# Kernel tuning notes

Hardware: AMD Instinct MI355X
Metric: run time of the kernel (lower is better)

The kernel has to match this reference:

```python
import jax, jax.numpy as jnp
import numpy as np

N_NODES = 50000
N_EDGES = 640000
D_IN = 128
D_HID = 128
D_OUT = 128
N_GRAPHS = 64


def gcn_conv(x, edge_index, W, b, n_nodes):
    """PyG GCNConv: D^{-1/2} (A + I) D^{-1/2} X W + b (unit edge weights)."""
    src, dst = edge_index[0], edge_index[1]
    h = x @ W  # [N, d_out]
    # degree counts target-side edges plus the self loop
    deg = jax.ops.segment_sum(jnp.ones_like(dst, dtype=h.dtype), dst,
                              num_segments=n_nodes) + 1.0
    dinv = jax.lax.rsqrt(deg)  # deg >= 1 so always finite
    norm = dinv[src] * dinv[dst]  # [E]
    msg = h[src] * norm[:, None]  # gather + scale  [E, d_out]
    agg = jax.ops.segment_sum(msg, dst, num_segments=n_nodes)
    # self-loop contribution: norm_ii = dinv_i^2
    agg = agg + h * (dinv * dinv)[:, None]
    return agg + b


def global_mean_pool(x, batch, n_graphs):
    sums = jax.ops.segment_sum(x, batch, num_segments=n_graphs)
    cnt = jax.ops.segment_sum(jnp.ones((x.shape[0],), dtype=x.dtype), batch,
                              num_segments=n_graphs)
    return sums / jnp.maximum(cnt, 1.0)[:, None]


def setup_inputs() -> dict:
    key = jax.random.key(0)
    k = jax.random.split(key, 8)
    x = jax.random.normal(k[0], (N_NODES, D_IN), dtype=jnp.float32)
    edge_index = jax.random.randint(k[1], (2, N_EDGES), 0, N_NODES, dtype=jnp.int64)
    batch = jnp.sort(jax.random.randint(k[2], (N_NODES,), 0, N_GRAPHS, dtype=jnp.int64))
    s1 = 1.0 / np.sqrt(D_IN)
    s2 = 1.0 / np.sqrt(D_HID)
    W1 = jax.random.uniform(k[3], (D_IN, D_HID), jnp.float32, -s1, s1)
    b1 = jnp.zeros((D_HID,), jnp.float32)
    W2 = jax.random.uniform(k[4], (D_HID, D_OUT), jnp.float32, -s2, s2)
    b2 = jnp.zeros((D_OUT,), jnp.float32)
    return {"x": x, "edge_index": edge_index, "batch": batch,
            "W1": W1, "b1": b1, "W2": W2, "b2": b2}


def reference(x, edge_index, batch, W1, b1, W2, b2):
    n = x.shape[0]
    h = jax.nn.relu(gcn_conv(x, edge_index, W1, b1, n))
    h = gcn_conv(h, edge_index, W2, b2, n)
    return global_mean_pool(h, batch, N_GRAPHS)
```

## Files before the change

kernel.cpp:

```cpp
#include <hip/hip_runtime.h>


#define D 128
#define NGRAPH 64
#define SCAN_B 1024
#define AGG_BLOCKS 2048

typedef _Float16 h16x2 __attribute__((ext_vector_type(2)));
typedef _Float16 f16x8 __attribute__((ext_vector_type(8)));
typedef float    f32x4 __attribute__((ext_vector_type(4)));

__device__ __forceinline__ float2 h2f(unsigned u) {
    h16x2 h = __builtin_bit_cast(h16x2, u);
    return make_float2((float)h.x, (float)h.y);
}
__device__ __forceinline__ unsigned f2h(float x, float y) {
    h16x2 h;
    h.x = (_Float16)x;
    h.y = (_Float16)y;
    return __builtin_bit_cast(unsigned, h);
}

__global__ void zero_out_kernel(float* __restrict__ out, int n) {
    int i = blockIdx.x * blockDim.x + threadIdx.x;
    if (i < n) out[i] = 0.f;
}

__global__ __launch_bounds__(256) void conv_count_kernel(const float* __restrict__ X,
                                                         _Float16* __restrict__ Xh,
                                                         const float* __restrict__ W1,
                                                         _Float16* __restrict__ WB,
                                                         const int* __restrict__ ei,
                                                         int* __restrict__ deg,
                                                         int N, int E, int cb) {
    int b = (int)blockIdx.x;
    if (b < cb) {
        int idx = b * 256 + (int)threadIdx.x;
        int total = N * (D / 4);
        if (idx < total) {
            float4 v = ((const float4*)X)[idx];
            uint2 o;
            o.x = f2h(v.x, v.y);
            o.y = f2h(v.z, v.w);
            ((uint2*)Xh)[idx] = o;
        }
        return;
    }
    if (b < cb + 8) {
        int idx = (b - cb) * 256 + (int)threadIdx.x;
        int lane = idx & 63;
        int nt   = (idx >> 6) & 7;
        int kt   = idx >> 9;
        int col  = nt * 16 + (lane & 15);
        int krow = kt * 32 + (lane >> 4) * 8;
#pragma unroll
        for (int j = 0; j < 8; ++j)
            WB[idx * 8 + j] = (_Float16)W1[(krow + j) * D + col];
        return;
    }
    int e = (b - cb - 8) * 256 + (int)threadIdx.x;
    if (e < E) {
        int d = ei[E + e];
        if (d >= 0 && d < N) atomicAdd(&deg[d], 1);
    }
}

__global__ __launch_bounds__(SCAN_B) void block_scan_kernel(const int* __restrict__ deg,
                                                            int* __restrict__ rowstart,
                                                            int* __restrict__ bsum,
                                                            float* __restrict__ dinv,
                                                            int N) {
    __shared__ int sc[SCAN_B];
    int t = threadIdx.x;
    int i = blockIdx.x * SCAN_B + t;
    int orig = (i < N) ? deg[i] : 0;
    int v = orig;
    sc[t] = v;
    __syncthreads();
    for (int off = 1; off < SCAN_B; off <<= 1) {
        int add = (t >= off) ? sc[t - off] : 0;
        __syncthreads();
        v += add;
        sc[t] = v;
        __syncthreads();
    }
    if (i < N) {
        rowstart[i] = v - orig;
        dinv[i]     = rsqrtf((float)orig + 1.0f);
    }
    if (t == SCAN_B - 1) bsum[blockIdx.x] = v;
}

__global__ __launch_bounds__(SCAN_B) void finalize_scan_kernel(const int* __restrict__ bsum,
                                                               int* __restrict__ rowstart,
                                                               int* __restrict__ cursor,
                                                               int N, int nblk, int E) {
    __shared__ int s_off;
    if (threadIdx.x < 64) {
        int lane = (int)threadIdx.x;
        int v = (lane < nblk && lane < (int)blockIdx.x) ? bsum[lane] : 0;
        for (int off = 32; off > 0; off >>= 1) v += __shfl_down(v, off);
        if (lane == 0) s_off = v;
    }
    __syncthreads();
    int i = blockIdx.x * SCAN_B + threadIdx.x;
    if (i < N) {
        int rs = rowstart[i] + s_off;
        rowstart[i] = rs;
        cursor[i]   = rs;
    }
    if (blockIdx.x == 0 && threadIdx.x == 0) rowstart[N] = E;
}

__global__ __launch_bounds__(256) void gemm_fill_kernel(const _Float16* __restrict__ Xh,
                                                        const _Float16* __restrict__ WB,
                                                        const float* __restrict__ dinv,
                                                        _Float16* __restrict__ Gh,
                                                        const int* __restrict__ ei,
                                                        int* __restrict__ cursor,
                                                        int* __restrict__ colidx,
                                                        int N, int E, int gb) {
    if ((int)blockIdx.x >= gb) {
        int e = ((int)blockIdx.x - gb) * 256 + (int)threadIdx.x;
        if (e < E) {
            int d = ei[E + e];
            if (d >= 0 && d < N) {
                int slot = atomicAdd(&cursor[d], 1);
                if (slot >= 0 && slot < E) {
                    int s = ei[e];
                    colidx[slot] = min(max(s, 0), N - 1);
                }
            }
        }
        return;
    }

    int t = (int)threadIdx.x;
    int wave = t >> 6, lane = t & 63;
    int mbase = blockIdx.x * 64 + wave * 16;
    int arow  = mbase + (lane & 15);
    if (arow >= N) arow = N - 1;
    int kgrp  = lane >> 4;

    f16x8 afrag[4];
#pragma unroll
    for (int kt = 0; kt < 4; ++kt) {
        uint4 u = *(const uint4*)(Xh + (size_t)arow * D + kt * 32 + kgrp * 8);
        afrag[kt] = __builtin_bit_cast(f16x8, u);
    }
    f32x4 acc[8];
#pragma unroll
    for (int nt = 0; nt < 8; ++nt) acc[nt] = (f32x4){0.f, 0.f, 0.f, 0.f};
#pragma unroll
    for (int kt = 0; kt < 4; ++kt) {
#pragma unroll
        for (int nt = 0; nt < 8; ++nt) {
            uint4 u = *(const uint4*)(WB + (((kt * 8 + nt) * 64 + lane) * 8));
            f16x8 bfrag = __builtin_bit_cast(f16x8, u);
            acc[nt] = __builtin_amdgcn_mfma_f32_16x16x32_f16(afrag[kt], bfrag, acc[nt], 0, 0, 0);
        }
    }
    int r0 = mbase + kgrp * 4;
#pragma unroll
    for (int r = 0; r < 4; ++r) {
        int row = r0 + r;
        if (row < N) {
            float dv = dinv[row];
#pragma unroll
            for (int nt = 0; nt < 8; ++nt)
                Gh[(size_t)row * D + nt * 16 + (lane & 15)] = (_Float16)(dv * acc[nt][r]);
        }
    }
}

__global__ __launch_bounds__(256) void agg1_kernel(const unsigned* __restrict__ Gh,
                                                   const int* __restrict__ rowstart,
                                                   const int* __restrict__ colidx,
                                                   const float* __restrict__ dinv,
                                                   const float* __restrict__ b1,
                                                   unsigned* __restrict__ Hh,
                                                   int N, int chunk) {
    int gid  = blockIdx.x * 4 + (threadIdx.x >> 6);
    int lane = threadIdx.x & 63;
    int i0 = gid * chunk, i1 = min(i0 + chunk, N);
    float bx = b1[2 * lane], by = b1[2 * lane + 1];
    for (int i = i0; i < i1; ++i) {
        float di = dinv[i];
        float2 acc = h2f(Gh[(size_t)i * (D / 2) + lane]);
        int e0 = rowstart[i], e1 = rowstart[i + 1];
        int e = e0;
        for (; e + 7 < e1; e += 8) {
            unsigned u[8];
#pragma unroll
            for (int j = 0; j < 8; ++j)
                u[j] = Gh[(size_t)colidx[e + j] * (D / 2) + lane];
#pragma unroll
            for (int j = 0; j < 8; ++j) {
                float2 v = h2f(u[j]);
                acc.x += v.x;
                acc.y += v.y;
            }
        }
        for (; e + 3 < e1; e += 4) {
            unsigned u[4];
#pragma unroll
            for (int j = 0; j < 4; ++j)
                u[j] = Gh[(size_t)colidx[e + j] * (D / 2) + lane];
#pragma unroll
            for (int j = 0; j < 4; ++j) {
                float2 v = h2f(u[j]);
                acc.x += v.x;
                acc.y += v.y;
            }
        }
        for (; e < e1; ++e) {
            float2 v = h2f(Gh[(size_t)colidx[e] * (D / 2) + lane]);
            acc.x += v.x;
            acc.y += v.y;
        }
        float hx = fmaxf(fmaf(di, acc.x, bx), 0.f) * di;
        float hy = fmaxf(fmaf(di, acc.y, by), 0.f) * di;
        Hh[(size_t)i * (D / 2) + lane] = f2h(hx, hy);
    }
}

__global__ __launch_bounds__(256) void agg2_pool_kernel(const unsigned* __restrict__ Hh,
                                                        const int* __restrict__ rowstart,
                                                        const int* __restrict__ colidx,
                                                        const float* __restrict__ dinv,
                                                        const int* __restrict__ batch,
                                                        float* __restrict__ pool,
                                                        int N, int chunk) {
    int gid  = blockIdx.x * 4 + (threadIdx.x >> 6);
    int lane = threadIdx.x & 63;
    int i0 = gid * chunk, i1 = min(i0 + chunk, N);
    if (i0 >= N) return;

    float2 pa = make_float2(0.f, 0.f);
    int cur = min(max(batch[i0], 0), NGRAPH - 1);
    for (int i = i0; i < i1; ++i) {
        float di = dinv[i];
        float2 a = h2f(Hh[(size_t)i * (D / 2) + lane]);
        int e0 = rowstart[i], e1 = rowstart[i + 1];
        int e = e0;
        for (; e + 7 < e1; e += 8) {
            unsigned u[8];
#pragma unroll
            for (int j = 0; j < 8; ++j)
                u[j] = Hh[(size_t)colidx[e + j] * (D / 2) + lane];
#pragma unroll
            for (int j = 0; j < 8; ++j) {
                float2 v = h2f(u[j]);
                a.x += v.x;
                a.y += v.y;
            }
        }
        for (; e + 3 < e1; e += 4) {
            unsigned u[4];
#pragma unroll
            for (int j = 0; j < 4; ++j)
                u[j] = Hh[(size_t)colidx[e + j] * (D / 2) + lane];
#pragma unroll
            for (int j = 0; j < 4; ++j) {
                float2 v = h2f(u[j]);
                a.x += v.x;
                a.y += v.y;
            }
        }
        for (; e < e1; ++e) {
            float2 v = h2f(Hh[(size_t)colidx[e] * (D / 2) + lane]);
            a.x += v.x;
            a.y += v.y;
        }
        int b = min(max(batch[i], 0), NGRAPH - 1);
        if (b != cur) {
            atomicAdd(&pool[(size_t)cur * D + 2 * lane], pa.x);
            atomicAdd(&pool[(size_t)cur * D + 2 * lane + 1], pa.y);
            pa = make_float2(0.f, 0.f);
            cur = b;
        }
        pa.x = fmaf(di, a.x, pa.x);
        pa.y = fmaf(di, a.y, pa.y);
    }
    atomicAdd(&pool[(size_t)cur * D + 2 * lane], pa.x);
    atomicAdd(&pool[(size_t)cur * D + 2 * lane + 1], pa.y);
}

__device__ __forceinline__ int lbound(const int* __restrict__ a, int n, int v) {
    int lo = 0, hi = n;
    while (lo < hi) {
        int m = (lo + hi) >> 1;
        if (a[m] < v) lo = m + 1; else hi = m;
    }
    return lo;
}

__global__ void final_gemm_kernel(const float* __restrict__ pool,
                                  const int* __restrict__ batch,
                                  const float* __restrict__ W2,
                                  const float* __restrict__ b2,
                                  float* __restrict__ out, int N) {
    int g = blockIdx.x, o = threadIdx.x;
    int s = lbound(batch, N, g);
    int e = lbound(batch, N, g + 1);
    float inv_cnt = 1.0f / fmaxf((float)(e - s), 1.0f);
    float acc = 0.f;
#pragma unroll 4
    for (int k = 0; k < D; ++k)
        acc = fmaf(pool[g * D + k], W2[k * D + o], acc);
    out[g * D + o] = acc * inv_cnt + b2[o];
}


extern "C" void kernel_launch(void* const* d_in, const int* in_sizes, int n_in,
                              void* d_out, int out_size, void* d_ws, size_t ws_size,
                              hipStream_t stream) {
    const float* x     = (const float*)d_in[0];
    const int*   ei    = (const int*)  d_in[1];
    const int*   batch = (const int*)  d_in[2];
    const float* W1    = (const float*)d_in[3];
    const float* b1    = (const float*)d_in[4];
    const float* W2    = (const float*)d_in[5];
    const float* b2    = (const float*)d_in[6];
    float* out = (float*)d_out;

    const int N = in_sizes[0] / D;
    const int E = in_sizes[1] / 2;
    const int nblk = (N + SCAN_B - 1) / SCAN_B;

    char* ws = (char*)d_ws;
    size_t off = 0;
    auto carve = [&](size_t bytes) {
        size_t o = off;
        off = (off + bytes + 255) & ~(size_t)255;
        return o;
    };
    size_t o_deg      = carve((size_t)N * 4);
    size_t o_pool     = carve((size_t)NGRAPH * D * 4);
    size_t zspan      = off;
    size_t o_rowstart = carve((size_t)(N + 1) * 4);
    size_t o_cursor   = carve((size_t)(N + 1) * 4);
    size_t o_dinv     = carve((size_t)N * 4);
    size_t o_colidx   = carve((size_t)E * 4);
    size_t o_bsum     = carve((size_t)64 * 4);
    size_t o_xh       = carve((size_t)N * D * 2);
    size_t o_wb       = carve((size_t)D * D * 2);
    size_t o_gh       = carve((size_t)N * D * 2);
    size_t o_hh       = carve((size_t)N * D * 2);
    size_t need = off;

    if (ws_size < need) {
        zero_out_kernel<<<(out_size + 255) / 256, 256, 0, stream>>>(out, out_size);
        return;
    }

    int*       deg      = (int*)      (ws + o_deg);
    float*     pool     = (float*)    (ws + o_pool);
    int*       rowstart = (int*)      (ws + o_rowstart);
    int*       cursor   = (int*)      (ws + o_cursor);
    float*     dinv     = (float*)    (ws + o_dinv);
    int*       colidx   = (int*)      (ws + o_colidx);
    int*       bsum     = (int*)      (ws + o_bsum);
    _Float16*  Xh       = (_Float16*) (ws + o_xh);
    _Float16*  WB       = (_Float16*) (ws + o_wb);
    _Float16*  Gh       = (_Float16*) (ws + o_gh);
    _Float16*  Hh       = (_Float16*) (ws + o_hh);

    hipMemsetAsync(ws, 0, zspan, stream);

    int eb = (E + 255) / 256;
    int gb = (N + 63) / 64;
    int cb = (N * (D / 4) + 255) / 256;

    conv_count_kernel<<<cb + 8 + eb, 256, 0, stream>>>(x, Xh, W1, WB, ei, deg, N, E, cb);
    block_scan_kernel<<<nblk, SCAN_B, 0, stream>>>(deg, rowstart, bsum, dinv, N);
    finalize_scan_kernel<<<nblk, SCAN_B, 0, stream>>>(bsum, rowstart, cursor, N, nblk, E);
    gemm_fill_kernel<<<gb + eb, 256, 0, stream>>>(Xh, WB, dinv, Gh, ei, cursor,
                                                  colidx, N, E, gb);

    int groups = AGG_BLOCKS * 4;
    int chunk  = (N + groups - 1) / groups;
    agg1_kernel<<<AGG_BLOCKS, 256, 0, stream>>>((const unsigned*)Gh, rowstart, colidx,
                                                dinv, b1, (unsigned*)Hh, N, chunk);
    agg2_pool_kernel<<<AGG_BLOCKS, 256, 0, stream>>>((const unsigned*)Hh, rowstart, colidx,
                                                     dinv, batch, pool, N, chunk);
    final_gemm_kernel<<<NGRAPH, D, 0, stream>>>(pool, batch, W2, b2, out, N);
}
```

Measured before the change: 224.2 us.

## Fold self-loops into CSR and flatten edge loop across rows in aggregation

Inserts each node's self-loop as the first entry of its CSR row, so the aggregation no longer issues a separate self-gather. Both aggregation kernels now walk all edges of a wave's row chunk as one flat stream in batches of 8, flushing a row's result when its edge range ends. This keeps gather batches full across short rows, since average degree is about 13, instead of dropping to 4-wide and scalar tails per row. It adds data-dependent inner while loops and branches inside the unrolled batch, which may cause wave divergence and extra register pressure.

```diff
diff --git a/kernel.cpp b/kernel.cpp
--- a/kernel.cpp
+++ b/kernel.cpp
@@ -73,7 +73,8 @@
     __shared__ int sc[SCAN_B];
     int t = threadIdx.x;
     int i = blockIdx.x * SCAN_B + t;
-    int orig = (i < N) ? deg[i] : 0;
+    int d0 = (i < N) ? deg[i] : 0;
+    int orig = (i < N) ? (d0 + 1) : 0;
     int v = orig;
     sc[t] = v;
     __syncthreads();
@@ -86,7 +87,7 @@
     }
     if (i < N) {
         rowstart[i] = v - orig;
-        dinv[i]     = rsqrtf((float)orig + 1.0f);
+        dinv[i]     = rsqrtf((float)d0 + 1.0f);
     }
     if (t == SCAN_B - 1) bsum[blockIdx.x] = v;
 }
@@ -94,7 +95,8 @@
 __global__ __launch_bounds__(SCAN_B) void finalize_scan_kernel(const int* __restrict__ bsum,
                                                                int* __restrict__ rowstart,
                                                                int* __restrict__ cursor,
-                                                               int N, int nblk, int E) {
+                                                               int* __restrict__ colidx,
+                                                               int N, int nblk, int EN) {
     __shared__ int s_off;
     if (threadIdx.x < 64) {
         int lane = (int)threadIdx.x;
@@ -107,9 +109,10 @@
     if (i < N) {
         int rs = rowstart[i] + s_off;
         rowstart[i] = rs;
-        cursor[i]   = rs;
-    }
-    if (blockIdx.x == 0 && threadIdx.x == 0) rowstart[N] = E;
+        cursor[i]   = rs + 1;
+        colidx[rs]  = i;
+    }
+    if (blockIdx.x == 0 && threadIdx.x == 0) rowstart[N] = EN;
 }
 
 __global__ __launch_bounds__(256) void gemm_fill_kernel(const _Float16* __restrict__ Xh,
@@ -119,14 +122,14 @@
                                                         const int* __restrict__ ei,
                                                         int* __restrict__ cursor,
                                                         int* __restrict__ colidx,
-                                                        int N, int E, int gb) {
+                                                        int N, int E, int EN, int gb) {
     if ((int)blockIdx.x >= gb) {
         int e = ((int)blockIdx.x - gb) * 256 + (int)threadIdx.x;
         if (e < E) {
             int d = ei[E + e];
             if (d >= 0 && d < N) {
                 int slot = atomicAdd(&cursor[d], 1);
-                if (slot >= 0 && slot < E) {
+                if (slot >= 0 && slot < EN) {
                     int s = ei[e];
                     colidx[slot] = min(max(s, 0), N - 1);
                 }
@@ -183,44 +186,60 @@
     int gid  = blockIdx.x * 4 + (threadIdx.x >> 6);
     int lane = threadIdx.x & 63;
     int i0 = gid * chunk, i1 = min(i0 + chunk, N);
+    if (i0 >= N) return;
     float bx = b1[2 * lane], by = b1[2 * lane + 1];
-    for (int i = i0; i < i1; ++i) {
-        float di = dinv[i];
-        float2 acc = h2f(Gh[(size_t)i * (D / 2) + lane]);
-        int e0 = rowstart[i], e1 = rowstart[i + 1];
-        int e = e0;
-        for (; e + 7 < e1; e += 8) {
-            unsigned u[8];
-#pragma unroll
-            for (int j = 0; j < 8; ++j)
-                u[j] = Gh[(size_t)colidx[e + j] * (D / 2) + lane];
-#pragma unroll
-            for (int j = 0; j < 8; ++j) {
-                float2 v = h2f(u[j]);
-                acc.x += v.x;
-                acc.y += v.y;
+
+    int i    = i0;
+    int eEnd = rowstart[i + 1];
+    int e    = rowstart[i0];
+    int eTot = rowstart[i1];
+    float2 acc = make_float2(0.f, 0.f);
+
+    while (e + 8 <= eTot) {
+        int s[8];
+        unsigned u[8];
+#pragma unroll
+        for (int j = 0; j < 8; ++j) s[j] = colidx[e + j];
+#pragma unroll
+        for (int j = 0; j < 8; ++j) u[j] = Gh[(size_t)s[j] * (D / 2) + lane];
+#pragma unroll
+        for (int j = 0; j < 8; ++j) {
+            while (e + j >= eEnd) {
+                float di = dinv[i];
+                float hx = fmaxf(fmaf(di, acc.x, bx), 0.f) * di;
+                float hy = fmaxf(fmaf(di, acc.y, by), 0.f) * di;
+                Hh[(size_t)i * (D / 2) + lane] = f2h(hx, hy);
+                acc = make_float2(0.f, 0.f);
+                ++i;
+                eEnd = rowstart[i + 1];
             }
-        }
-        for (; e + 3 < e1; e += 4) {
-            unsigned u[4];
-#pragma unroll
-            for (int j = 0; j < 4; ++j)
-                u[j] = Gh[(size_t)colidx[e + j] * (D / 2) + lane];
-#pragma unroll
-            for (int j = 0; j < 4; ++j) {
-                float2 v = h2f(u[j]);
-                acc.x += v.x;
-                acc.y += v.y;
-            }
-        }
-        for (; e < e1; ++e) {
-            float2 v = h2f(Gh[(size_t)colidx[e] * (D / 2) + lane]);
+            float2 v = h2f(u[j]);
             acc.x += v.x;
             acc.y += v.y;
         }
+        e += 8;
+    }
+    while (e < eTot) {
+        while (e >= eEnd) {
+            float di = dinv[i];
+            float hx = fmaxf(fmaf(di, acc.x, bx), 0.f) * di;
+            float hy = fmaxf(fmaf(di, acc.y, by), 0.f) * di;
+            Hh[(size_t)i * (D / 2) + lane] = f2h(hx, hy);
+            acc = make_float2(0.f, 0.f);
+            ++i;
+            eEnd = rowstart[i + 1];
+        }
+        float2 v = h2f(Gh[(size_t)colidx[e] * (D / 2) + lane]);
+        acc.x += v.x;
+        acc.y += v.y;
+        ++e;
+    }
+    for (; i < i1; ++i) {
+        float di = dinv[i];
         float hx = fmaxf(fmaf(di, acc.x, bx), 0.f) * di;
         float hy = fmaxf(fmaf(di, acc.y, by), 0.f) * di;
         Hh[(size_t)i * (D / 2) + lane] = f2h(hx, hy);
+        acc = make_float2(0.f, 0.f);
     }
 }
 
@@ -236,42 +255,67 @@
     int i0 = gid * chunk, i1 = min(i0 + chunk, N);
     if (i0 >= N) return;
 
-    float2 pa = make_float2(0.f, 0.f);
+    int i    = i0;
+    int eEnd = rowstart[i + 1];
+    int e    = rowstart[i0];
+    int eTot = rowstart[i1];
+    float2 acc = make_float2(0.f, 0.f);
+    float2 pa  = make_float2(0.f, 0.f);
     int cur = min(max(batch[i0], 0), NGRAPH - 1);
-    for (int i = i0; i < i1; ++i) {
+
+    while (e + 8 <= eTot) {
+        int s[8];
+        unsigned u[8];
+#pragma unroll
+        for (int j = 0; j < 8; ++j) s[j] = colidx[e + j];
+#pragma unroll
+        for (int j = 0; j < 8; ++j) u[j] = Hh[(size_t)s[j] * (D / 2) + lane];
+#pragma unroll
+        for (int j = 0; j < 8; ++j) {
+            while (e + j >= eEnd) {
+                float di = dinv[i];
+                int b = min(max(batch[i], 0), NGRAPH - 1);
+                if (b != cur) {
+                    atomicAdd(&pool[(size_t)cur * D + 2 * lane], pa.x);
+                    atomicAdd(&pool[(size_t)cur * D + 2 * lane + 1], pa.y);
+                    pa = make_float2(0.f, 0.f);
+                    cur = b;
+                }
+                pa.x = fmaf(di, acc.x, pa.x);
+                pa.y = fmaf(di, acc.y, pa.y);
+                acc = make_float2(0.f, 0.f);
+                ++i;
+                eEnd = rowstart[i + 1];
+            }
+            float2 v = h2f(u[j]);
+            acc.x += v.x;
+            acc.y += v.y;
+        }
+        e += 8;
+    }
+    while (e < eTot) {
+        while (e >= eEnd) {
+            float di = dinv[i];
+            int b = min(max(batch[i], 0), NGRAPH - 1);
+            if (b != cur) {
+                atomicAdd(&pool[(size_t)cur * D + 2 * lane], pa.x);
+                atomicAdd(&pool[(size_t)cur * D + 2 * lane + 1], pa.y);
+                pa = make_float2(0.f, 0.f);
+                cur = b;
+            }
+            pa.x = fmaf(di, acc.x, pa.x);
+            pa.y = fmaf(di, acc.y, pa.y);
+            acc = make_float2(0.f, 0.f);
+            ++i;
+            eEnd = rowstart[i + 1];
+        }
+        float2 v = h2f(Hh[(size_t)colidx[e] * (D / 2) + lane]);
+        acc.x += v.x;
+        acc.y += v.y;
+        ++e;
+    }
+    for (; i < i1; ++i) {
         float di = dinv[i];
-        float2 a = h2f(Hh[(size_t)i * (D / 2) + lane]);
-        int e0 = rowstart[i], e1 = rowstart[i + 1];
-        int e = e0;
-        for (; e + 7 < e1; e += 8) {
-            unsigned u[8];
-#pragma unroll
-            for (int j = 0; j < 8; ++j)
-                u[j] = Hh[(size_t)colidx[e + j] * (D / 2) + lane];
-#pragma unroll
-            for (int j = 0; j < 8; ++j) {
-                float2 v = h2f(u[j]);
-                a.x += v.x;
-                a.y += v.y;
-            }
-        }
-        for (; e + 3 < e1; e += 4) {
-            unsigned u[4];
-#pragma unroll
-            for (int j = 0; j < 4; ++j)
-                u[j] = Hh[(size_t)colidx[e + j] * (D / 2) + lane];
-#pragma unroll
-            for (int j = 0; j < 4; ++j) {
-                float2 v = h2f(u[j]);
-                a.x += v.x;
-                a.y += v.y;
-            }
-        }
-        for (; e < e1; ++e) {
-            float2 v = h2f(Hh[(size_t)colidx[e] * (D / 2) + lane]);
-            a.x += v.x;
-            a.y += v.y;
-        }
         int b = min(max(batch[i], 0), NGRAPH - 1);
         if (b != cur) {
             atomicAdd(&pool[(size_t)cur * D + 2 * lane], pa.x);
@@ -279,8 +323,9 @@
             pa = make_float2(0.f, 0.f);
             cur = b;
         }
-        pa.x = fmaf(di, a.x, pa.x);
-        pa.y = fmaf(di, a.y, pa.y);
+        pa.x = fmaf(di, acc.x, pa.x);
+        pa.y = fmaf(di, acc.y, pa.y);
+        acc = make_float2(0.f, 0.f);
     }
     atomicAdd(&pool[(size_t)cur * D + 2 * lane], pa.x);
     atomicAdd(&pool[(size_t)cur * D + 2 * lane + 1], pa.y);
@@ -326,6 +371,7 @@
 
     const int N = in_sizes[0] / D;
     const int E = in_sizes[1] / 2;
+    const int EN = E + N;
     const int nblk = (N + SCAN_B - 1) / SCAN_B;
 
     char* ws = (char*)d_ws;
@@ -341,7 +387,7 @@
     size_t o_rowstart = carve((size_t)(N + 1) * 4);
     size_t o_cursor   = carve((size_t)(N + 1) * 4);
     size_t o_dinv     = carve((size_t)N * 4);
-    size_t o_colidx   = carve((size_t)E * 4);
+    size_t o_colidx   = carve((size_t)EN * 4);
     size_t o_bsum     = carve((size_t)64 * 4);
     size_t o_xh       = carve((size_t)N * D * 2);
     size_t o_wb       = carve((size_t)D * D * 2);
@@ -374,9 +420,10 @@
 
     conv_count_kernel<<<cb + 8 + eb, 256, 0, stream>>>(x, Xh, W1, WB, ei, deg, N, E, cb);
     block_scan_kernel<<<nblk, SCAN_B, 0, stream>>>(deg, rowstart, bsum, dinv, N);
-    finalize_scan_kernel<<<nblk, SCAN_B, 0, stream>>>(bsum, rowstart, cursor, N, nblk, E);
+    finalize_scan_kernel<<<nblk, SCAN_B, 0, stream>>>(bsum, rowstart, cursor, colidx,
+                                                      N, nblk, EN);
     gemm_fill_kernel<<<gb + eb, 256, 0, stream>>>(Xh, WB, dinv, Gh, ei, cursor,
-                                                  colidx, N, E, gb);
+                                                  colidx, N, E, EN, gb);
 
     int groups = AGG_BLOCKS * 4;
     int chunk  = (N + groups - 1) / groups;
```

Measured after the change: 232.7 us. +3.8%, slower.
